# Kernel optimization log

Measured on AMD Instinct MI355X. Metric: run time of the kernel, lower is better.

The kernel has to match this reference:

```python
import jax, jax.numpy as jnp
import numpy as np
import math

HID_DIM = 1024
NUM_HEADS = 8
QK_DIM = HID_DIM // 8  # 128 total, 16 per head


def setup_inputs() -> dict:
    key = jax.random.key(0)
    ks = jax.random.split(key, 7)
    B, M, C = 4, 2048, HID_DIM
    gain = math.sqrt(2.0)  # calculate_gain('relu')

    def xavier(k, fan_in, fan_out):
        std = gain * math.sqrt(2.0 / (fan_in + fan_out))
        a = math.sqrt(3.0) * std
        return jax.random.uniform(k, (fan_out, fan_in), jnp.float32, -a, a)

    x = jax.random.normal(ks[0], (B, M, C), jnp.float32)
    Wq = xavier(ks[1], C, QK_DIM)   # [out, in] like torch Linear
    Wk = xavier(ks[2], C, QK_DIM)
    Wv = xavier(ks[3], C, C)
    bq = jnp.zeros((QK_DIM,), jnp.float32)
    bk = jnp.zeros((QK_DIM,), jnp.float32)
    bv = jnp.zeros((C,), jnp.float32)
    gamma = jnp.zeros((1,), jnp.float32)
    return {"x": x, "Wq": Wq, "bq": bq, "Wk": Wk, "bk": bk,
            "Wv": Wv, "bv": bv, "gamma": gamma}


def reference(x, Wq, bq, Wk, bk, Wv, bv, gamma):
    B, M, C = x.shape
    H = NUM_HEADS
    dqk = QK_DIM // H   # per-head qk dim = 16
    dv = C // H         # per-head v dim = 128
    q = (x @ Wq.T + bq).reshape(B, M, H, dqk)  # [B,M,H,dqk]
    k = (x @ Wk.T + bk).reshape(B, M, H, dqk)
    v = (x @ Wv.T + bv).reshape(B, M, H, dv)
    scores = jnp.einsum('bmhd,bnhd->bhmn', q, k) / math.sqrt(dqk)
    scores = jnp.where(scores >= 0, scores, 0.2 * scores)  # LeakyReLU(0.2)
    beta = jax.nn.softmax(scores, axis=-1)                 # [B,H,M,M]
    out = jnp.einsum('bhmn,bnhd->bmhd', beta, v).reshape(B, M, C)
    return gamma * out + x
```

## Files before the change

### kernel.cpp

```cpp
#include <hip/hip_runtime.h>
#include <hip/hip_bf16.h>

typedef __bf16 bf16_t;
typedef __bf16 bf16x8 __attribute__((ext_vector_type(8)));
typedef float f32x4 __attribute__((ext_vector_type(4)));
typedef float f32x16 __attribute__((ext_vector_type(16)));

#define MTOT 8192
#define CDIM 1024
#define HEADS 8
#define DV 128
#define QKD 128
#define SEQ 2048
#define QSCALE 0.3606737602222409f

struct alignas(8) B4 { bf16_t a, b, c, d; };

__device__ inline bf16x8 cvt8(float4 a, float4 b) {
    bf16x8 v = { (bf16_t)a.x, (bf16_t)a.y, (bf16_t)a.z, (bf16_t)a.w,
                 (bf16_t)b.x, (bf16_t)b.y, (bf16_t)b.z, (bf16_t)b.w };
    return v;
}

__device__ inline void gl_lds16(const bf16_t* g, bf16_t* l) {
    __builtin_amdgcn_global_load_lds(
        (const __attribute__((address_space(1))) void*)g,
        (__attribute__((address_space(3))) void*)l, 16, 0, 0);
}

__global__ __launch_bounds__(256) void cvt_x(
    const float* __restrict__ src, bf16_t* __restrict__ dst, int n8)
{
    int i = blockIdx.x * blockDim.x + threadIdx.x;
    if (i >= n8) return;
    const float4* s = reinterpret_cast<const float4*>(src) + (size_t)i * 2;
    reinterpret_cast<bf16x8*>(dst)[i] = cvt8(s[0], s[1]);
}

__global__ __launch_bounds__(256) void cvt_w(
    const float* __restrict__ Wq, const float* __restrict__ Wk,
    const float* __restrict__ Wv, bf16_t* __restrict__ Wb)
{
    int i = blockIdx.x * blockDim.x + threadIdx.x;
    const float* src;
    if (i < 16384)       src = Wq + (size_t)i * 8;
    else if (i < 32768)  src = Wk + (size_t)(i - 16384) * 8;
    else                 src = Wv + (size_t)(i - 32768) * 8;
    const float4* s = reinterpret_cast<const float4*>(src);
    reinterpret_cast<bf16x8*>(Wb)[i] = cvt8(s[0], s[1]);
}

__global__ __launch_bounds__(256) void qkv_gemm3(
    const bf16_t* __restrict__ Xb, const bf16_t* __restrict__ Wb,
    const float* __restrict__ bq, const float* __restrict__ bk,
    const float* __restrict__ bv,
    bf16_t* __restrict__ Qw, bf16_t* __restrict__ Kw, bf16_t* __restrict__ Vt)
{
    __shared__ bf16_t As[128][64];
    __shared__ bf16_t Bs[128][64];

    const int tid = threadIdx.x;
    const int w = tid >> 6, l = tid & 63;
    const int c = l & 15, q = l >> 4;
    const int rw = w & 1, cw = w >> 1;
    const int bx = blockIdx.x;
    const int m0 = blockIdx.y * 128;

    const bf16_t* Arow = Xb + (size_t)(m0 + w * 8 + (l >> 3)) * CDIM + (l & 7) * 8;
    const bf16_t* Brow = Wb + (size_t)(bx * 128 + w * 8 + (l >> 3)) * CDIM + (l & 7) * 8;

    f32x4 acc[16] = {};

    for (int k0 = 0; k0 < CDIM; k0 += 64) {
        __syncthreads();
        #pragma unroll
        for (int i = 0; i < 4; ++i) {
            gl_lds16(Arow + k0 + (size_t)i * 32 * CDIM, &As[i * 32 + w * 8][0]);
            gl_lds16(Brow + k0 + (size_t)i * 32 * CDIM, &Bs[i * 32 + w * 8][0]);
        }
        __syncthreads();
        #pragma unroll
        for (int kk = 0; kk < 2; ++kk) {
            bf16x8 af[4], bfr[4];
            #pragma unroll
            for (int mt = 0; mt < 4; ++mt)
                af[mt] = *(const bf16x8*)&As[rw * 64 + mt * 16 + c][kk * 32 + q * 8];
            #pragma unroll
            for (int nt = 0; nt < 4; ++nt)
                bfr[nt] = *(const bf16x8*)&Bs[cw * 64 + nt * 16 + c][kk * 32 + q * 8];
            #pragma unroll
            for (int mt = 0; mt < 4; ++mt)
                #pragma unroll
                for (int nt = 0; nt < 4; ++nt)
                    acc[mt * 4 + nt] = __builtin_amdgcn_mfma_f32_16x16x32_bf16(
                        af[mt], bfr[nt], acc[mt * 4 + nt], 0, 0, 0);
        }
    }

    #pragma unroll
    for (int mt = 0; mt < 4; ++mt)
        #pragma unroll
        for (int nt = 0; nt < 4; ++nt) {
            const int cl = cw * 64 + nt * 16 + c;
            f32x4 a = acc[mt * 4 + nt];
            const int mg = m0 + rw * 64 + mt * 16 + q * 4;
            if (bx == 0) {
                const float bb = bq[cl];
                #pragma unroll
                for (int r = 0; r < 4; ++r)
                    Qw[(size_t)(mg + r) * QKD + cl] = (bf16_t)((a[r] + bb) * QSCALE);
            } else if (bx == 1) {
                const float bb = bk[cl];
                #pragma unroll
                for (int r = 0; r < 4; ++r)
                    Kw[(size_t)(mg + r) * QKD + cl] = (bf16_t)(a[r] + bb);
            } else {
                const int h = bx - 2;
                const float bb = bv[h * DV + cl];
                const int bidx = mg >> 11, ml = mg & 2047;
                B4 v{ (bf16_t)(a[0] + bb), (bf16_t)(a[1] + bb),
                      (bf16_t)(a[2] + bb), (bf16_t)(a[3] + bb) };
                *(B4*)(Vt + ((size_t)(bidx * HEADS + h) * DV + cl) * SEQ + ml) = v;
            }
        }
}

__global__ __launch_bounds__(256, 2) void qkv_gemm2(
    const float* __restrict__ X,
    const float* __restrict__ Wq, const float* __restrict__ bq,
    const float* __restrict__ Wk, const float* __restrict__ bk,
    const float* __restrict__ Wv, const float* __restrict__ bv,
    bf16_t* __restrict__ Qw, bf16_t* __restrict__ Kw, bf16_t* __restrict__ Vt)
{
    __shared__ alignas(16) bf16_t As[128][72];
    __shared__ alignas(16) bf16_t Bs[128][72];

    const int tid  = threadIdx.x;
    const int lane = tid & 63, wave = tid >> 6;
    const int c = lane & 15, q = lane >> 4;
    const int rw = wave & 1, cw = wave >> 1;
    const int m0 = blockIdx.y * 128;
    const int nt_idx = blockIdx.x;

    const float* W; const float* bias;
    if (nt_idx == 0)      { W = Wq; bias = bq; }
    else if (nt_idx == 1) { W = Wk; bias = bk; }
    else { W = Wv + (size_t)(nt_idx - 2) * DV * CDIM; bias = bv + (nt_idx - 2) * DV; }

    const int srow = tid >> 1, sseg = tid & 1;
    const int swr = (srow >> 3) & 3;
    const float* ax = X + (size_t)(m0 + srow) * CDIM + sseg * 32;
    const float* bxp = W + (size_t)srow * CDIM + sseg * 32;

    f32x4 acc[16] = {};

    for (int k0 = 0; k0 < CDIM; k0 += 64) {
        __syncthreads();
        #pragma unroll
        for (int i = 0; i < 4; ++i) {
            const int ph = (sseg * 4 + i) ^ swr;
            *(bf16x8*)&As[srow][ph * 8] = cvt8(*(const float4*)(ax + k0 + i * 8),
                                               *(const float4*)(ax + k0 + i * 8 + 4));
            *(bf16x8*)&Bs[srow][ph * 8] = cvt8(*(const float4*)(bxp + k0 + i * 8),
                                               *(const float4*)(bxp + k0 + i * 8 + 4));
        }
        __syncthreads();
        #pragma unroll
        for (int kk = 0; kk < 2; ++kk) {
            bf16x8 af[4], bfr[4];
            #pragma unroll
            for (int mt = 0; mt < 4; ++mt) {
                const int row = rw * 64 + mt * 16 + c;
                af[mt] = *(const bf16x8*)&As[row][((kk * 4 + q) ^ ((row >> 3) & 3)) * 8];
            }
            #pragma unroll
            for (int nt = 0; nt < 4; ++nt) {
                const int row = cw * 64 + nt * 16 + c;
                bfr[nt] = *(const bf16x8*)&Bs[row][((kk * 4 + q) ^ ((row >> 3) & 3)) * 8];
            }
            #pragma unroll
            for (int mt = 0; mt < 4; ++mt)
                #pragma unroll
                for (int nt = 0; nt < 4; ++nt)
                    acc[mt * 4 + nt] = __builtin_amdgcn_mfma_f32_16x16x32_bf16(
                        af[mt], bfr[nt], acc[mt * 4 + nt], 0, 0, 0);
        }
    }

    #pragma unroll
    for (int mt = 0; mt < 4; ++mt)
        #pragma unroll
        for (int nt = 0; nt < 4; ++nt) {
            const int col = cw * 64 + nt * 16 + c;
            const float bb = bias[col];
            f32x4 a = acc[mt * 4 + nt];
            const int mg = m0 + rw * 64 + mt * 16 + q * 4;
            if (nt_idx == 0) {
                #pragma unroll
                for (int r = 0; r < 4; ++r)
                    Qw[(size_t)(mg + r) * QKD + col] = (bf16_t)((a[r] + bb) * QSCALE);
            } else if (nt_idx == 1) {
                #pragma unroll
                for (int r = 0; r < 4; ++r)
                    Kw[(size_t)(mg + r) * QKD + col] = (bf16_t)(a[r] + bb);
            } else {
                const int h = nt_idx - 2;
                const int bidx = mg >> 11, ml = mg & 2047;
                B4 v{ (bf16_t)(a[0] + bb), (bf16_t)(a[1] + bb),
                      (bf16_t)(a[2] + bb), (bf16_t)(a[3] + bb) };
                *(B4*)(Vt + ((size_t)(bidx * HEADS + h) * DV + col) * SEQ + ml) = v;
            }
        }
}

__global__ __launch_bounds__(256, 2) void attn3(
    const bf16_t* __restrict__ Q, const bf16_t* __restrict__ K,
    const bf16_t* __restrict__ Vt, const float* __restrict__ X,
    const float* __restrict__ gptr, float* __restrict__ out)
{
    __shared__ alignas(16) bf16_t Vs[128][72];
    __shared__ alignas(16) bf16_t Ps[4][32][72];

    const int tid  = threadIdx.x;
    const int lane = tid & 63, wave = tid >> 6;
    const int c5 = lane & 31, q1 = lane >> 5;
    const int bh = blockIdx.y;
    const int b = bh >> 3, h = bh & 7;
    const int mbase = blockIdx.x * 128 + wave * 32;

    const bf16x8 qf = *(const bf16x8*)(
        Q + (size_t)(b * SEQ + mbase + c5) * QKD + h * 16 + q1 * 8);

    float li = 0.f;
    f32x16 o[4] = {};

    const bf16_t* Vhead = Vt + (size_t)(b * HEADS + h) * DV * SEQ;
    const bf16_t* Kbase = K + (size_t)(b * SEQ) * QKD + h * 16;

    const int sdv = tid >> 1, sseg = tid & 1;
    const int swv = (sdv >> 3) & 7;
    const int swp = (c5 >> 3) & 3;

    bf16x8 vreg[4], kreg[2];
    {
        const bf16_t* src = Vhead + (size_t)sdv * SEQ + sseg * 32;
        #pragma unroll
        for (int i = 0; i < 4; ++i) vreg[i] = *(const bf16x8*)(src + i * 8);
        #pragma unroll
        for (int blk = 0; blk < 2; ++blk)
            kreg[blk] = *(const bf16x8*)(Kbase + (size_t)(blk * 32 + c5) * QKD + q1 * 8);
    }

    for (int n0 = 0; n0 < SEQ; n0 += 64) {
        __syncthreads();
        #pragma unroll
        for (int i = 0; i < 4; ++i) {
            const int ph = (sseg * 4 + i) ^ swv;
            *(bf16x8*)&Vs[sdv][ph * 8] = vreg[i];
        }
        __syncthreads();

        const bf16x8 k0f = kreg[0], k1f = kreg[1];
        if (n0 + 64 < SEQ) {
            const bf16_t* src = Vhead + (size_t)sdv * SEQ + n0 + 64 + sseg * 32;
            #pragma unroll
            for (int i = 0; i < 4; ++i) vreg[i] = *(const bf16x8*)(src + i * 8);
            #pragma unroll
            for (int blk = 0; blk < 2; ++blk)
                kreg[blk] = *(const bf16x8*)(
                    Kbase + (size_t)(n0 + 64 + blk * 32 + c5) * QKD + q1 * 8);
        }

        #pragma unroll
        for (int blk = 0; blk < 2; ++blk) {
            f32x16 z = {};
            f32x16 s = __builtin_amdgcn_mfma_f32_32x32x16_bf16(
                blk ? k1f : k0f, qf, z, 0, 0, 0);
            #pragma unroll
            for (int rr = 0; rr < 4; ++rr) {
                float p[4];
                #pragma unroll
                for (int j = 0; j < 4; ++j) {
                    const float sv = s[rr * 4 + j];
                    const float e = __builtin_amdgcn_exp2f(fmaxf(sv, 0.2f * sv));
                    p[j] = e;
                    li += e;
                }
                const int ph = (blk * 4 + rr) ^ swp;
                B4 pv{ (bf16_t)p[0], (bf16_t)p[1], (bf16_t)p[2], (bf16_t)p[3] };
                *(B4*)&Ps[wave][c5][ph * 8 + q1 * 4] = pv;
            }
        }

        #pragma unroll
        for (int kt = 0; kt < 4; ++kt) {
            const int phA = (kt * 2 + q1) ^ swp;
            const bf16x8 pa = *(const bf16x8*)&Ps[wave][c5][phA * 8];
            #pragma unroll
            for (int dvt = 0; dvt < 4; ++dvt) {
                const int dv = dvt * 32 + c5;
                const int phB = (kt * 2 + q1) ^ ((dv >> 3) & 7);
                const bf16x8 vb = *(const bf16x8*)&Vs[dv][phB * 8];
                o[dvt] = __builtin_amdgcn_mfma_f32_32x32x16_bf16(pa, vb, o[dvt], 0, 0, 0);
            }
        }
    }

    li += __shfl_xor(li, 32);
    const float inv = 1.f / li;
    const float g = gptr[0];

    #pragma unroll
    for (int dvt = 0; dvt < 4; ++dvt)
        #pragma unroll
        for (int r = 0; r < 16; ++r) {
            const int row = (r & 3) + 8 * (r >> 2) + 4 * q1;
            const float linv = __shfl(inv, row);
            const size_t idx = (size_t)(b * SEQ + mbase + row) * CDIM
                             + h * DV + dvt * 32 + c5;
            out[idx] = g * (o[dvt][r] * linv) + X[idx];
        }
}

extern "C" void kernel_launch(void* const* d_in, const int* in_sizes, int n_in,
                              void* d_out, int out_size, void* d_ws, size_t ws_size,
                              hipStream_t stream) {
    const float* X  = (const float*)d_in[0];
    const float* Wq = (const float*)d_in[1];
    const float* bq = (const float*)d_in[2];
    const float* Wk = (const float*)d_in[3];
    const float* bk = (const float*)d_in[4];
    const float* Wv = (const float*)d_in[5];
    const float* bv = (const float*)d_in[6];
    const float* g  = (const float*)d_in[7];
    float* out = (float*)d_out;

    dim3 blk(256);
    const size_t big_elems = (size_t)MTOT * CDIM + 1280 * CDIM
                           + (size_t)MTOT * QKD * 2 + (size_t)MTOT * CDIM;
    const size_t big_ws = big_elems * sizeof(bf16_t);

    if (ws_size >= big_ws) {
        bf16_t* Xb = (bf16_t*)d_ws;
        bf16_t* Wb = Xb + (size_t)MTOT * CDIM;
        bf16_t* Qw = Wb + (size_t)1280 * CDIM;
        bf16_t* Kw = Qw + (size_t)MTOT * QKD;
        bf16_t* Vt = Kw + (size_t)MTOT * QKD;

        hipLaunchKernelGGL(cvt_x, dim3(MTOT * CDIM / 8 / 256), blk, 0, stream,
                           X, Xb, MTOT * CDIM / 8);
        hipLaunchKernelGGL(cvt_w, dim3(1280 * CDIM / 8 / 256), blk, 0, stream,
                           Wq, Wk, Wv, Wb);
        hipLaunchKernelGGL(qkv_gemm3, dim3(10, 64), blk, 0, stream,
                           Xb, Wb, bq, bk, bv, Qw, Kw, Vt);
        hipLaunchKernelGGL(attn3, dim3(SEQ / 128, 32), blk, 0, stream,
                           Qw, Kw, Vt, X, g, out);
    } else {
        bf16_t* Qw = (bf16_t*)d_ws;
        bf16_t* Kw = Qw + (size_t)MTOT * QKD;
        bf16_t* Vt = Kw + (size_t)MTOT * QKD;
        hipLaunchKernelGGL(qkv_gemm2, dim3(10, 64), blk, 0, stream,
                           X, Wq, bq, Wk, bk, Wv, bv, Qw, Kw, Vt);
        hipLaunchKernelGGL(attn3, dim3(SEQ / 128, 32), blk, 0, stream,
                           Qw, Kw, Vt, X, g, out);
    }
}
```

Measured before the change: 214.7 us.

## Double-buffer V tiles in attention and remap blocks for XCD-local L2 reuse

The attention kernel now keeps two LDS buffers for V and prefetches V tiles two steps ahead in registers. This cuts one barrier per iteration and lets the next tile's LDS store overlap the current compute. The loop is unrolled by two with s_setprio raised around the PV MFMA section. Both the QKV GEMM and the attention kernel remap their linear block index so that blocks on the same XCD share heads and rows, aiming for better L2 locality. The cost is more registers and LDS per block, which may lower occupancy.

After: 210.7 us. Within noise of the previous version (-1.9%).

```diff
diff --git a/kernel.cpp b/kernel.cpp
--- a/kernel.cpp
+++ b/kernel.cpp
@@ -63,8 +63,11 @@
     const int w = tid >> 6, l = tid & 63;
     const int c = l & 15, q = l >> 4;
     const int rw = w & 1, cw = w >> 1;
-    const int bx = blockIdx.x;
-    const int m0 = blockIdx.y * 128;
+
+    const int lin = blockIdx.x + 10 * blockIdx.y;
+    const int xcd = lin & 7, jj = lin >> 3;
+    const int bx = jj % 10;
+    const int m0 = (xcd * 8 + jj / 10) * 128;
 
     const bf16_t* Arow = Xb + (size_t)(m0 + w * 8 + (l >> 3)) * CDIM + (l & 7) * 8;
     const bf16_t* Brow = Wb + (size_t)(bx * 128 + w * 8 + (l >> 3)) * CDIM + (l & 7) * 8;
@@ -218,15 +221,19 @@
     const bf16_t* __restrict__ Vt, const float* __restrict__ X,
     const float* __restrict__ gptr, float* __restrict__ out)
 {
-    __shared__ alignas(16) bf16_t Vs[128][72];
+    __shared__ alignas(16) bf16_t Vs[2][128][72];
     __shared__ alignas(16) bf16_t Ps[4][32][72];
 
     const int tid  = threadIdx.x;
     const int lane = tid & 63, wave = tid >> 6;
     const int c5 = lane & 31, q1 = lane >> 5;
-    const int bh = blockIdx.y;
+
+    const int lin = blockIdx.x + (SEQ / 128) * blockIdx.y;
+    const int xcd = lin & 7, jj = lin >> 3;
+    const int bh = xcd * 4 + (jj >> 4);
+    const int qt = jj & 15;
     const int b = bh >> 3, h = bh & 7;
-    const int mbase = blockIdx.x * 128 + wave * 32;
+    const int mbase = qt * 128 + wave * 32;
 
     const bf16x8 qf = *(const bf16x8*)(
         Q + (size_t)(b * SEQ + mbase + c5) * QKD + h * 16 + q1 * 8);
@@ -241,68 +248,142 @@
     const int swv = (sdv >> 3) & 7;
     const int swp = (c5 >> 3) & 3;
 
-    bf16x8 vreg[4], kreg[2];
+    bf16x8 vA[4], vB[4], kA[2], kB[2];
+
     {
-        const bf16_t* src = Vhead + (size_t)sdv * SEQ + sseg * 32;
-        #pragma unroll
-        for (int i = 0; i < 4; ++i) vreg[i] = *(const bf16x8*)(src + i * 8);
-        #pragma unroll
-        for (int blk = 0; blk < 2; ++blk)
-            kreg[blk] = *(const bf16x8*)(Kbase + (size_t)(blk * 32 + c5) * QKD + q1 * 8);
-    }
-
-    for (int n0 = 0; n0 < SEQ; n0 += 64) {
-        __syncthreads();
+        const bf16_t* s0 = Vhead + (size_t)sdv * SEQ + sseg * 32;
+        #pragma unroll
+        for (int i = 0; i < 4; ++i) vA[i] = *(const bf16x8*)(s0 + i * 8);
+        const bf16_t* s1 = s0 + 64;
+        #pragma unroll
+        for (int i = 0; i < 4; ++i) vB[i] = *(const bf16x8*)(s1 + i * 8);
+        #pragma unroll
+        for (int blk = 0; blk < 2; ++blk) {
+            kA[blk] = *(const bf16x8*)(Kbase + (size_t)(blk * 32 + c5) * QKD + q1 * 8);
+            kB[blk] = *(const bf16x8*)(Kbase + (size_t)(64 + blk * 32 + c5) * QKD + q1 * 8);
+        }
         #pragma unroll
         for (int i = 0; i < 4; ++i) {
             const int ph = (sseg * 4 + i) ^ swv;
-            *(bf16x8*)&Vs[sdv][ph * 8] = vreg[i];
-        }
-        __syncthreads();
-
-        const bf16x8 k0f = kreg[0], k1f = kreg[1];
-        if (n0 + 64 < SEQ) {
-            const bf16_t* src = Vhead + (size_t)sdv * SEQ + n0 + 64 + sseg * 32;
-            #pragma unroll
-            for (int i = 0; i < 4; ++i) vreg[i] = *(const bf16x8*)(src + i * 8);
-            #pragma unroll
-            for (int blk = 0; blk < 2; ++blk)
-                kreg[blk] = *(const bf16x8*)(
-                    Kbase + (size_t)(n0 + 64 + blk * 32 + c5) * QKD + q1 * 8);
-        }
-
-        #pragma unroll
-        for (int blk = 0; blk < 2; ++blk) {
-            f32x16 z = {};
-            f32x16 s = __builtin_amdgcn_mfma_f32_32x32x16_bf16(
-                blk ? k1f : k0f, qf, z, 0, 0, 0);
-            #pragma unroll
-            for (int rr = 0; rr < 4; ++rr) {
-                float p[4];
-                #pragma unroll
-                for (int j = 0; j < 4; ++j) {
-                    const float sv = s[rr * 4 + j];
-                    const float e = __builtin_amdgcn_exp2f(fmaxf(sv, 0.2f * sv));
-                    p[j] = e;
-                    li += e;
+            *(bf16x8*)&Vs[0][sdv][ph * 8] = vA[i];
+        }
+        const bf16_t* s2 = s0 + 128;
+        #pragma unroll
+        for (int i = 0; i < 4; ++i) vA[i] = *(const bf16x8*)(s2 + i * 8);
+    }
+
+    #pragma unroll 1
+    for (int t = 0; t < 32; t += 2) {
+        {
+            __syncthreads();
+            #pragma unroll
+            for (int i = 0; i < 4; ++i) {
+                const int ph = (sseg * 4 + i) ^ swv;
+                *(bf16x8*)&Vs[1][sdv][ph * 8] = vB[i];
+            }
+            {
+                const int vt = (t + 3 < 32) ? t + 3 : 31;
+                const int kt2 = (t + 2 < 32) ? t + 2 : 31;
+                const bf16_t* src = Vhead + (size_t)sdv * SEQ + vt * 64 + sseg * 32;
+                #pragma unroll
+                for (int i = 0; i < 4; ++i) vB[i] = *(const bf16x8*)(src + i * 8);
+                const bf16x8 k0f = kA[0], k1f = kA[1];
+                #pragma unroll
+                for (int blk = 0; blk < 2; ++blk)
+                    kA[blk] = *(const bf16x8*)(
+                        Kbase + (size_t)(kt2 * 64 + blk * 32 + c5) * QKD + q1 * 8);
+
+                #pragma unroll
+                for (int blk = 0; blk < 2; ++blk) {
+                    f32x16 z = {};
+                    f32x16 s = __builtin_amdgcn_mfma_f32_32x32x16_bf16(
+                        blk ? k1f : k0f, qf, z, 0, 0, 0);
+                    #pragma unroll
+                    for (int rr = 0; rr < 4; ++rr) {
+                        float p[4];
+                        #pragma unroll
+                        for (int j = 0; j < 4; ++j) {
+                            const float sv = s[rr * 4 + j];
+                            const float e = __builtin_amdgcn_exp2f(fmaxf(sv, 0.2f * sv));
+                            p[j] = e;
+                            li += e;
+                        }
+                        const int ph = (blk * 4 + rr) ^ swp;
+                        B4 pv{ (bf16_t)p[0], (bf16_t)p[1], (bf16_t)p[2], (bf16_t)p[3] };
+                        *(B4*)&Ps[wave][c5][ph * 8 + q1 * 4] = pv;
+                    }
                 }
-                const int ph = (blk * 4 + rr) ^ swp;
-                B4 pv{ (bf16_t)p[0], (bf16_t)p[1], (bf16_t)p[2], (bf16_t)p[3] };
-                *(B4*)&Ps[wave][c5][ph * 8 + q1 * 4] = pv;
-            }
-        }
-
-        #pragma unroll
-        for (int kt = 0; kt < 4; ++kt) {
-            const int phA = (kt * 2 + q1) ^ swp;
-            const bf16x8 pa = *(const bf16x8*)&Ps[wave][c5][phA * 8];
-            #pragma unroll
-            for (int dvt = 0; dvt < 4; ++dvt) {
-                const int dv = dvt * 32 + c5;
-                const int phB = (kt * 2 + q1) ^ ((dv >> 3) & 7);
-                const bf16x8 vb = *(const bf16x8*)&Vs[dv][phB * 8];
-                o[dvt] = __builtin_amdgcn_mfma_f32_32x32x16_bf16(pa, vb, o[dvt], 0, 0, 0);
-            }
+            }
+            __builtin_amdgcn_s_setprio(1);
+            #pragma unroll
+            for (int kt = 0; kt < 4; ++kt) {
+                const int phA = (kt * 2 + q1) ^ swp;
+                const bf16x8 pa = *(const bf16x8*)&Ps[wave][c5][phA * 8];
+                #pragma unroll
+                for (int dvt = 0; dvt < 4; ++dvt) {
+                    const int dv = dvt * 32 + c5;
+                    const int phB = (kt * 2 + q1) ^ ((dv >> 3) & 7);
+                    const bf16x8 vb = *(const bf16x8*)&Vs[0][dv][phB * 8];
+                    o[dvt] = __builtin_amdgcn_mfma_f32_32x32x16_bf16(pa, vb, o[dvt], 0, 0, 0);
+                }
+            }
+            __builtin_amdgcn_s_setprio(0);
+        }
+        {
+            const int u = t + 1;
+            __syncthreads();
+            #pragma unroll
+            for (int i = 0; i < 4; ++i) {
+                const int ph = (sseg * 4 + i) ^ swv;
+                *(bf16x8*)&Vs[0][sdv][ph * 8] = vA[i];
+            }
+            {
+                const int vt = (u + 3 < 32) ? u + 3 : 31;
+                const int kt2 = (u + 2 < 32) ? u + 2 : 31;
+                const bf16_t* src = Vhead + (size_t)sdv * SEQ + vt * 64 + sseg * 32;
+                #pragma unroll
+                for (int i = 0; i < 4; ++i) vA[i] = *(const bf16x8*)(src + i * 8);
+                const bf16x8 k0f = kB[0], k1f = kB[1];
+                #pragma unroll
+                for (int blk = 0; blk < 2; ++blk)
+                    kB[blk] = *(const bf16x8*)(
+                        Kbase + (size_t)(kt2 * 64 + blk * 32 + c5) * QKD + q1 * 8);
+
+                #pragma unroll
+                for (int blk = 0; blk < 2; ++blk) {
+                    f32x16 z = {};
+                    f32x16 s = __builtin_amdgcn_mfma_f32_32x32x16_bf16(
+                        blk ? k1f : k0f, qf, z, 0, 0, 0);
+                    #pragma unroll
+                    for (int rr = 0; rr < 4; ++rr) {
+                        float p[4];
+                        #pragma unroll
+                        for (int j = 0; j < 4; ++j) {
+                            const float sv = s[rr * 4 + j];
+                            const float e = __builtin_amdgcn_exp2f(fmaxf(sv, 0.2f * sv));
+                            p[j] = e;
+                            li += e;
+                        }
+                        const int ph = (blk * 4 + rr) ^ swp;
+                        B4 pv{ (bf16_t)p[0], (bf16_t)p[1], (bf16_t)p[2], (bf16_t)p[3] };
+                        *(B4*)&Ps[wave][c5][ph * 8 + q1 * 4] = pv;
+                    }
+                }
+            }
+            __builtin_amdgcn_s_setprio(1);
+            #pragma unroll
+            for (int kt = 0; kt < 4; ++kt) {
+                const int phA = (kt * 2 + q1) ^ swp;
+                const bf16x8 pa = *(const bf16x8*)&Ps[wave][c5][phA * 8];
+                #pragma unroll
+                for (int dvt = 0; dvt < 4; ++dvt) {
+                    const int dv = dvt * 32 + c5;
+                    const int phB = (kt * 2 + q1) ^ ((dv >> 3) & 7);
+                    const bf16x8 vb = *(const bf16x8*)&Vs[1][dv][phB * 8];
+                    o[dvt] = __builtin_amdgcn_mfma_f32_32x32x16_bf16(pa, vb, o[dvt], 0, 0, 0);
+                }
+            }
+            __builtin_amdgcn_s_setprio(0);
         }
     }
 
```
